# Performance work log

Measured on AMD Instinct MI355X. Metric: run time of the kernel, lower is better.

The kernel has to match this reference:

```python
import jax, jax.numpy as jnp
import numpy as np
from jax import lax

C = 256        # CONV_DIM / hidden size
VOC = 97       # VOC_SIZE + 1
T_DEC = 25     # NUM_CHARS
N = 512        # number of rois
H_IN, W_IN = 8, 32
GROUPS = 32    # GroupNorm groups (detectron2 'GN' default)


def setup_inputs() -> dict:
    key = jax.random.key(0)
    ks = jax.random.split(key, 16)
    nrm = lambda k, shp, s=0.05: jax.random.normal(k, shp, dtype=jnp.float32) * s
    inp = {}
    inp['rois'] = jax.random.normal(ks[0], (N, C, H_IN, W_IN), dtype=jnp.float32)
    inp['targets'] = jax.random.randint(ks[1], (N, T_DEC), 0, VOC)
    inp['conv1_w'] = nrm(ks[2], (C, C, 3, 3))
    inp['gn1_s'] = jnp.ones((C,), jnp.float32); inp['gn1_b'] = jnp.zeros((C,), jnp.float32)
    inp['conv2_w'] = nrm(ks[3], (C, C, 3, 3))
    inp['gn2_s'] = jnp.ones((C,), jnp.float32); inp['gn2_b'] = jnp.zeros((C,), jnp.float32)
    inp['lstm_wih_f'] = nrm(ks[4], (4 * C, C)); inp['lstm_whh_f'] = nrm(ks[5], (4 * C, C))
    inp['lstm_bih_f'] = jnp.zeros((4 * C,), jnp.float32); inp['lstm_bhh_f'] = jnp.zeros((4 * C,), jnp.float32)
    inp['lstm_wih_b'] = nrm(ks[6], (4 * C, C)); inp['lstm_whh_b'] = nrm(ks[7], (4 * C, C))
    inp['lstm_bih_b'] = jnp.zeros((4 * C,), jnp.float32); inp['lstm_bhh_b'] = jnp.zeros((4 * C,), jnp.float32)
    inp['emb_w'] = nrm(ks[8], (C, 2 * C)); inp['emb_b'] = jnp.zeros((C,), jnp.float32)
    inp['att_emb'] = nrm(ks[9], (VOC, C), 1.0)
    inp['comb_w'] = nrm(ks[10], (C, 2 * C)); inp['comb_b'] = jnp.zeros((C,), jnp.float32)
    inp['gru_wih'] = nrm(ks[11], (3 * C, C)); inp['gru_whh'] = nrm(ks[12], (3 * C, C))
    inp['gru_bih'] = jnp.zeros((3 * C,), jnp.float32); inp['gru_bhh'] = jnp.zeros((3 * C,), jnp.float32)
    inp['out_w'] = nrm(ks[13], (VOC, C)); inp['out_b'] = jnp.zeros((VOC,), jnp.float32)
    inp['vat_w'] = nrm(ks[14], (1, C)); inp['vat_b'] = jnp.zeros((1,), jnp.float32)
    return inp


def group_norm(x, scale, bias, groups=GROUPS, eps=1e-5):
    n, c, h, w = x.shape
    xg = x.reshape(n, groups, c // groups, h, w)
    mu = xg.mean(axis=(2, 3, 4), keepdims=True)
    var = xg.var(axis=(2, 3, 4), keepdims=True)
    xg = (xg - mu) * lax.rsqrt(var + eps)
    return xg.reshape(n, c, h, w) * scale[None, :, None, None] + bias[None, :, None, None]


def lstm_dir(xs, w_ih, w_hh, b_ih, b_hh, reverse):
    # xs: (T, N, C); PyTorch LSTM gate order i, f, g, o
    n = xs.shape[1]; hdim = w_hh.shape[1]
    def step(carry, x):
        h, c = carry
        g = x @ w_ih.T + b_ih + h @ w_hh.T + b_hh
        i, f, gg, o = jnp.split(g, 4, axis=-1)
        c = jax.nn.sigmoid(f) * c + jax.nn.sigmoid(i) * jnp.tanh(gg)
        h = jax.nn.sigmoid(o) * jnp.tanh(c)
        return (h, c), h
    z = jnp.zeros((n, hdim), xs.dtype)
    _, hs = lax.scan(step, (z, z), xs, reverse=reverse)
    return hs


def reference(rois, targets, conv1_w, gn1_s, gn1_b, conv2_w, gn2_s, gn2_b,
              lstm_wih_f, lstm_whh_f, lstm_bih_f, lstm_bhh_f,
              lstm_wih_b, lstm_whh_b, lstm_bih_b, lstm_bhh_b,
              emb_w, emb_b, att_emb, comb_w, comb_b,
              gru_wih, gru_whh, gru_bih, gru_bhh, out_w, out_b, vat_w, vat_b):
    # ---- CRNN encoder ----
    def conv_gn_relu(x, w, s, b):
        y = lax.conv_general_dilated(x, w, window_strides=(2, 1),
                                     padding=((1, 1), (1, 1)),
                                     dimension_numbers=('NCHW', 'OIHW', 'NCHW'))
        return jax.nn.relu(group_norm(y, s, b))
    x = conv_gn_relu(rois, conv1_w, gn1_s, gn1_b)
    x = conv_gn_relu(x, conv2_w, gn2_s, gn2_b)
    x = x.mean(axis=2).transpose(2, 0, 1)            # (T=W, N, C)
    hf = lstm_dir(x, lstm_wih_f, lstm_whh_f, lstm_bih_f, lstm_bhh_f, False)
    hb = lstm_dir(x, lstm_wih_b, lstm_whh_b, lstm_bih_b, lstm_bhh_b, True)
    enc = jnp.concatenate([hf, hb], axis=-1) @ emb_w.T + emb_b   # (T, N, C)

    # ---- attention GRU decoder (training path, deterministic teacher forcing) ----
    n = enc.shape[1]
    dec_in = jnp.concatenate([jnp.zeros((n, 1), targets.dtype), targets[:, :-1]], axis=1).T  # (T_DEC, N)
    dec_tgt = targets.T                                                                        # (T_DEC, N)

    def dec_step(h, inp):
        tok, tgt = inp                       # (N,), (N,)
        emb = att_emb[tok]                   # (N, C); dropout disabled
        alpha = jnp.tanh(h[None] + enc)      # (T, N, C)
        scores = jnp.einsum('tnc,c->tn', alpha, vat_w[0]) + vat_b[0]
        aw = jax.nn.softmax(scores, axis=0)  # softmax over encoder time
        ctx = jnp.einsum('tn,tnc->nc', aw, enc)
        xin = jax.nn.relu(jnp.concatenate([emb, ctx], axis=1) @ comb_w.T + comb_b)
        gi = xin @ gru_wih.T + gru_bih
        gh = h @ gru_whh.T + gru_bhh
        ir, iz, inn = jnp.split(gi, 3, axis=1)
        hr, hz, hn = jnp.split(gh, 3, axis=1)
        r = jax.nn.sigmoid(ir + hr)
        z = jax.nn.sigmoid(iz + hz)
        ng = jnp.tanh(inn + r * hn)
        h_new = (1.0 - z) * ng + z * h
        logp = jax.nn.log_softmax(h_new @ out_w.T + out_b, axis=1)
        step_loss = -jnp.mean(jnp.take_along_axis(logp, tgt[:, None], axis=1))
        return h_new, step_loss

    h0 = jnp.zeros((n, C), enc.dtype)
    _, losses = lax.scan(dec_step, h0, (dec_in, dec_tgt))
    return losses.sum()
```

## Files before the change

kernel.cpp:

```cpp
#include <hip/hip_runtime.h>
#include <math.h>

#define NROI 512
#define CDIM 256
#define TENC 32
#define TDEC 25
#define VOCC 97

typedef unsigned short ushort_t;
typedef unsigned char uchar_t;
typedef __attribute__((ext_vector_type(8))) short short8v;
typedef __attribute__((ext_vector_type(4))) float float4v;

__device__ __forceinline__ float sigmoidf_(float x){
    x = fminf(fmaxf(x, -30.f), 30.f);
    return __builtin_amdgcn_rcpf(1.f + __expf(-x));
}
__device__ __forceinline__ float tanhf_(float x){
    x = fminf(fmaxf(x, -15.f), 15.f);
    float e = __expf(2.f * x);
    return (e - 1.f) * __builtin_amdgcn_rcpf(e + 1.f);
}
__device__ __forceinline__ ushort_t f2b(float f){
    unsigned u = __float_as_uint(f);
    u = u + 0x7fffu + ((u >> 16) & 1u);
    return (ushort_t)(u >> 16);
}
__device__ __forceinline__ float b2f(ushort_t h){
    return __uint_as_float(((unsigned)h) << 16);
}
__device__ __forceinline__ uchar_t f2fp8(float x){
    x = fminf(fmaxf(x, -448.f), 448.f);
    int p = __builtin_amdgcn_cvt_pk_fp8_f32(x, x, 0, false);
    return (uchar_t)(p & 0xff);
}

__global__ void convert_all_k(
    const float* c1s, const float* c2s, const float* wf, const float* wb,
    const float* hf, const float* hb, const float* em, const float* cb,
    const float* gi, const float* gh, const float* ow, const float* ob,
    const float* bif, const float* bhf, const float* bib, const float* bhb,
    ushort_t* d_c1, ushort_t* d_c2, ushort_t* d_wf, ushort_t* d_wb,
    uchar_t* d_hf8, uchar_t* d_hb8, ushort_t* d_em,
    ushort_t* d_cwL, uchar_t* d_cwR8,
    uchar_t* d_gi8, uchar_t* d_gh8, ushort_t* d_ow, float* d_ob,
    float* d_b2f, float* d_b2b)
{
    int i = blockIdx.x * 256 + threadIdx.x;
    if (i < 589824) {
        int co = i / 2304, rem = i % 2304, tap = rem >> 8, ci = rem & 255;
        d_c1[i] = f2b(c1s[co * 2304 + ci * 9 + tap]); return;
    }
    i -= 589824;
    if (i < 589824) {
        int co = i / 2304, rem = i % 2304, tap = rem >> 8, ci = rem & 255;
        d_c2[i] = f2b(c2s[co * 2304 + ci * 9 + tap]); return;
    }
    i -= 589824;
    if (i < 262144) { d_wf[i] = f2b(wf[i]); return; }  i -= 262144;
    if (i < 262144) { d_wb[i] = f2b(wb[i]); return; }  i -= 262144;
    if (i < 262144) { d_hf8[i] = f2fp8(hf[i]); return; }  i -= 262144;
    if (i < 262144) { d_hb8[i] = f2fp8(hb[i]); return; }  i -= 262144;
    if (i < 131072) { d_em[i] = f2b(em[i]); return; }  i -= 131072;
    if (i < 131072) {
        int col = i >> 9, rest = i & 511;
        float v = cb[i];
        if (rest < 256) d_cwL[col * 256 + rest] = f2b(v);
        else            d_cwR8[col * 256 + (rest - 256)] = f2fp8(v);
        return;
    }
    i -= 131072;
    if (i < 196608) { d_gi8[i] = f2fp8(gi[i]); return; }  i -= 196608;
    if (i < 196608) { d_gh8[i] = f2fp8(gh[i]); return; }  i -= 196608;
    if (i < 32768) {
        int r = i >> 8;
        d_ow[i] = (r < VOCC) ? f2b(ow[i - (r << 8) + r * 256]) : 0; return;
    }
    i -= 32768;
    if (i < 128) { d_ob[i] = (i < VOCC) ? ob[i] : 0.f; return; }  i -= 128;
    if (i < 1024) { d_b2f[i] = bif[i] + bhf[i]; return; }  i -= 1024;
    if (i < 1024) { d_b2b[i] = bib[i] + bhb[i]; return; }
}

__global__ void nchw2nhwc_k(const float* __restrict__ in, ushort_t* __restrict__ out)
{
    __shared__ float t[64][33];
    int b = blockIdx.x;
    int cb = b & 3, h = (b >> 2) & 7, n = b >> 5;
    const float* src = in + (((size_t)n * 256 + cb * 64) * 8 + h) * 32;
    int w = threadIdx.x & 31, cr = threadIdx.x >> 5;
    #pragma unroll
    for (int p = 0; p < 8; p++) {
        int c = p * 8 + cr;
        t[c][w] = src[(size_t)c * 256 + w];
    }
    __syncthreads();
    int c2 = threadIdx.x & 63, wr2 = threadIdx.x >> 6;
    ushort_t* dst = out + ((size_t)n * 8 + h) * 32 * 256 + cb * 64;
    #pragma unroll
    for (int q = 0; q < 8; q++) {
        int ww = q * 4 + wr2;
        dst[(size_t)ww * 256 + c2] = f2b(t[c2][ww]);
    }
}

__global__ void emb_gather_k(const int* __restrict__ targets, const float* __restrict__ att_emb,
                             ushort_t* __restrict__ EMB)
{
    int idx = blockIdx.x * 256 + threadIdx.x;
    int c = idx & 255;
    int n = (idx >> 8) & 511;
    int t = idx >> 17;
    int tok = (t == 0) ? 0 : targets[n * TDEC + t - 1];
    EMB[idx] = f2b(att_emb[tok * 256 + c]);
}

template<int OUTBF, int ACT>
__global__ void __launch_bounds__(256, 2)
mgemm_k(const ushort_t* __restrict__ A, const ushort_t* __restrict__ B,
        const float* __restrict__ bias, void* __restrict__ Cout,
        int M, int N, int K)
{
    __shared__ ushort_t As[128 * 40];
    __shared__ ushort_t Bs[128 * 40];
    const int tid = threadIdx.x;
    const int lane = tid & 63, wid = tid >> 6;
    const int wr = wid >> 1, wc = wid & 1;
    const int bm = blockIdx.y * 128, bn = blockIdx.x * 128;

    const int r0 = tid >> 2, c0 = tid & 3;
    const int r1 = r0 + 64;
    const size_t Ar0 = (size_t)(bm + r0) * K, Ar1 = (size_t)(bm + r1) * K;
    const size_t Br0 = (size_t)(bn + r0) * K, Br1 = (size_t)(bn + r1) * K;

    float4v acc[4][4];
    #pragma unroll
    for (int m = 0; m < 4; m++)
        #pragma unroll
        for (int n = 0; n < 4; n++) { float4v z = {0.f,0.f,0.f,0.f}; acc[m][n] = z; }

    short8v ra[2][2], rb[2][2];
    auto LOAD = [&](int b, int k0) {
        ra[b][0] = *(const short8v*)&A[Ar0 + k0 + c0 * 8];
        ra[b][1] = *(const short8v*)&A[Ar1 + k0 + c0 * 8];
        rb[b][0] = *(const short8v*)&B[Br0 + k0 + c0 * 8];
        rb[b][1] = *(const short8v*)&B[Br1 + k0 + c0 * 8];
    };
    auto STORE = [&](int b) {
        *(short8v*)&As[r0 * 40 + c0 * 8] = ra[b][0];
        *(short8v*)&As[r1 * 40 + c0 * 8] = ra[b][1];
        *(short8v*)&Bs[r0 * 40 + c0 * 8] = rb[b][0];
        *(short8v*)&Bs[r1 * 40 + c0 * 8] = rb[b][1];
    };
    const int lr = lane & 15, lk = lane >> 4;
    auto COMPUTE = [&]() {
        short8v af[4], bf[4];
        #pragma unroll
        for (int m = 0; m < 4; m++)
            af[m] = *(const short8v*)&As[(wr * 64 + m * 16 + lr) * 40 + lk * 8];
        #pragma unroll
        for (int n = 0; n < 4; n++)
            bf[n] = *(const short8v*)&Bs[(wc * 64 + n * 16 + lr) * 40 + lk * 8];
        #pragma unroll
        for (int m = 0; m < 4; m++)
            #pragma unroll
            for (int n = 0; n < 4; n++)
                acc[m][n] = __builtin_amdgcn_mfma_f32_16x16x32_bf16(af[m], bf[n], acc[m][n], 0, 0, 0);
    };

    LOAD(0, 0);
    for (int k0 = 0; k0 < K; k0 += 64) {
        __syncthreads();
        STORE(0);
        __syncthreads();
        LOAD(1, k0 + 32);
        COMPUTE();
        __syncthreads();
        STORE(1);
        __syncthreads();
        if (k0 + 64 < K) LOAD(0, k0 + 64);
        COMPUTE();
    }

    #pragma unroll
    for (int m = 0; m < 4; m++)
        #pragma unroll
        for (int n = 0; n < 4; n++)
            #pragma unroll
            for (int r = 0; r < 4; r++) {
                int row = bm + wr * 64 + m * 16 + lk * 4 + r;
                int col = bn + wc * 64 + n * 16 + lr;
                float v = acc[m][n][r];
                if (bias) v += bias[col];
                if (ACT == 1) v = fmaxf(v, 0.f);
                if (OUTBF) ((ushort_t*)Cout)[(size_t)row * N + col] = f2b(v);
                else       ((float*)   Cout)[(size_t)row * N + col] = v;
            }
}

__global__ void __launch_bounds__(256, 2)
cgemm_k(const ushort_t* __restrict__ in, const ushort_t* __restrict__ wt,
        ushort_t* __restrict__ out, int Hin, int hmask, int nshift)
{
    const int K = 2304;
    __shared__ ushort_t As[128 * 40];
    __shared__ ushort_t Bs[256 * 40];
    const int tid = threadIdx.x;
    const int lane = tid & 63, wv = tid >> 6;
    const int byy = (blockIdx.y & 7) * (gridDim.y >> 3) + (blockIdx.y >> 3);
    const int bm = byy * 128;

    const int r0 = tid >> 2, c0 = tid & 3;
    const int r1 = r0 + 64;
    const int row0 = bm + r0, row1 = bm + r1;
    const int wo0 = row0 & 31, wo1 = row1 & 31;
    const int hh0 = ((row0 >> 5) & hmask) * 2 - 1, hh1 = ((row1 >> 5) & hmask) * 2 - 1;
    const size_t base0 = (size_t)(row0 >> nshift) * Hin * 32 * 256;
    const size_t base1 = (size_t)(row1 >> nshift) * Hin * 32 * 256;
    size_t Br[4];
    #pragma unroll
    for (int j = 0; j < 4; j++) Br[j] = (size_t)(r0 + j * 64) * K;

    float4v acc[8][4];
    #pragma unroll
    for (int m = 0; m < 8; m++)
        #pragma unroll
        for (int n = 0; n < 4; n++) { float4v z = {0.f,0.f,0.f,0.f}; acc[m][n] = z; }

    short8v ra[2][2], rb[2][4];
    const short8v zv = {0,0,0,0,0,0,0,0};
    auto LOAD = [&](int b, int k0) {
        int tap = k0 >> 8;
        int kh = tap / 3, kw = tap - kh * 3;
        int ci = (k0 & 255) + c0 * 8;
        int hi0 = hh0 + kh, wi0 = wo0 - 1 + kw;
        int hi1 = hh1 + kh, wi1 = wo1 - 1 + kw;
        ra[b][0] = ((unsigned)hi0 < (unsigned)Hin && (unsigned)wi0 < 32u)
                 ? *(const short8v*)&in[base0 + ((size_t)hi0 * 32 + wi0) * 256 + ci] : zv;
        ra[b][1] = ((unsigned)hi1 < (unsigned)Hin && (unsigned)wi1 < 32u)
                 ? *(const short8v*)&in[base1 + ((size_t)hi1 * 32 + wi1) * 256 + ci] : zv;
        #pragma unroll
        for (int j = 0; j < 4; j++)
            rb[b][j] = *(const short8v*)&wt[Br[j] + k0 + c0 * 8];
    };
    auto STORE = [&](int b) {
        *(short8v*)&As[r0 * 40 + c0 * 8] = ra[b][0];
        *(short8v*)&As[r1 * 40 + c0 * 8] = ra[b][1];
        #pragma unroll
        for (int j = 0; j < 4; j++)
            *(short8v*)&Bs[(r0 + j * 64) * 40 + c0 * 8] = rb[b][j];
    };
    const int lr = lane & 15, lk = lane >> 4;
    auto COMPUTE = [&]() {
        short8v af[8];
        #pragma unroll
        for (int m = 0; m < 8; m++)
            af[m] = *(const short8v*)&As[(m * 16 + lr) * 40 + lk * 8];
        #pragma unroll
        for (int n = 0; n < 4; n++) {
            short8v bf = *(const short8v*)&Bs[(wv * 64 + n * 16 + lr) * 40 + lk * 8];
            #pragma unroll
            for (int m = 0; m < 8; m++)
                acc[m][n] = __builtin_amdgcn_mfma_f32_16x16x32_bf16(af[m], bf, acc[m][n], 0, 0, 0);
        }
    };

    LOAD(0, 0);
    for (int k0 = 0; k0 < K; k0 += 64) {
        __syncthreads();
        STORE(0);
        __syncthreads();
        LOAD(1, k0 + 32);
        COMPUTE();
        __syncthreads();
        STORE(1);
        __syncthreads();
        if (k0 + 64 < K) LOAD(0, k0 + 64);
        COMPUTE();
    }

    #pragma unroll
    for (int m = 0; m < 8; m++)
        #pragma unroll
        for (int n = 0; n < 4; n++)
            #pragma unroll
            for (int r = 0; r < 4; r++) {
                int row = bm + m * 16 + lk * 4 + r;
                int col = wv * 64 + n * 16 + lr;
                out[(size_t)row * 256 + col] = f2b(acc[m][n][r]);
            }
}

__device__ __forceinline__ void gn_stats(float sum, float sq, int len,
                                         float* rs, float* rq, float& mu, float& rstd)
{
    for (int o = 32; o > 0; o >>= 1) { sum += __shfl_down(sum, o); sq += __shfl_down(sq, o); }
    int wid = threadIdx.x >> 6, lane = threadIdx.x & 63;
    if (lane == 0) { rs[wid] = sum; rq[wid] = sq; }
    __syncthreads();
    if (threadIdx.x == 0) {
        float S = rs[0] + rs[1] + rs[2] + rs[3];
        float Q = rq[0] + rq[1] + rq[2] + rq[3];
        float m = S / len;
        rs[4] = m; rq[4] = rsqrtf(Q / len - m * m + 1e-5f);
    }
    __syncthreads();
    mu = rs[4]; rstd = rq[4];
}

__global__ void gn_nhwc_k(const ushort_t* __restrict__ y, ushort_t* __restrict__ x,
                          const float* __restrict__ s, const float* __restrict__ b, int HW)
{
    __shared__ float rs[8], rq[8];
    int blk = blockIdx.x; int g = blk & 31; int n = blk >> 5;
    const ushort_t* p = y + (size_t)n * HW * 256 + g * 8;
    ushort_t* q = x + (size_t)n * HW * 256 + g * 8;
    int len = HW * 8;
    float sum = 0.f, sq = 0.f;
    for (int e = threadIdx.x; e < len; e += 256) {
        int hw = e >> 3, c = e & 7;
        float v = b2f(p[hw * 256 + c]);
        sum += v; sq += v * v;
    }
    float mu, rstd;
    gn_stats(sum, sq, len, rs, rq, mu, rstd);
    for (int e = threadIdx.x; e < len; e += 256) {
        int hw = e >> 3, c = e & 7;
        float v = (b2f(p[hw * 256 + c]) - mu) * rstd * s[g * 8 + c] + b[g * 8 + c];
        q[hw * 256 + c] = f2b(fmaxf(v, 0.f));
    }
}

__global__ void gn_pool_k(const ushort_t* __restrict__ y, ushort_t* __restrict__ xT,
                          const float* __restrict__ s, const float* __restrict__ b)
{
    __shared__ float rs[8], rq[8];
    int blk = blockIdx.x; int g = blk & 31; int n = blk >> 5;
    const ushort_t* p = y + (size_t)n * 64 * 256 + g * 8;
    float sum = 0.f, sq = 0.f;
    for (int e = threadIdx.x; e < 512; e += 256) {
        int hw = e >> 3, c = e & 7;
        float v = b2f(p[hw * 256 + c]);
        sum += v; sq += v * v;
    }
    float mu, rstd;
    gn_stats(sum, sq, 512, rs, rq, mu, rstd);
    int w = threadIdx.x >> 3, c = threadIdx.x & 7;
    float sc = s[g * 8 + c], bb = b[g * 8 + c];
    float v0 = (b2f(p[(size_t)w * 256 + c]) - mu) * rstd * sc + bb;
    float v1 = (b2f(p[(size_t)(32 + w) * 256 + c]) - mu) * rstd * sc + bb;
    float pooled = 0.5f * (fmaxf(v0, 0.f) + fmaxf(v1, 0.f));
    xT[((size_t)w * 512 + n) * 256 + g * 8 + c] = f2b(pooled);
}

__global__ void __launch_bounds__(512, 1)
lstm_persist_k(const ushort_t* __restrict__ XG,
               const uchar_t* __restrict__ whF8, const uchar_t* __restrict__ whB8,
               ushort_t* __restrict__ hcat)
{
    __shared__ __align__(16) uchar_t hf8[16][264];
    __shared__ float gL[16][1028];
    const int blk = blockIdx.x;
    const int dir = blk >> 5;
    const int r0  = (blk & 31) * 16;
    const uchar_t* W = dir ? whB8 : whF8;
    const int tid = threadIdx.x, lane = tid & 63, wv = tid >> 6;
    const int lr = lane & 15, lk = lane >> 4;
    const float4v z4 = {0.f, 0.f, 0.f, 0.f};

    long pw[8][8];
    #pragma unroll
    for (int j = 0; j < 8; j++) {
        int col0 = (j * 8 + wv) * 16;
        #pragma unroll
        for (int kf = 0; kf < 8; kf++)
            pw[j][kf] = *(const long*)&W[(size_t)(col0 + lr) * 256 + kf * 32 + lk * 8];
    }

    for (int i = tid; i < 16 * 264; i += 512) ((uchar_t*)hf8)[i] = 0;
    float creg[8];
    #pragma unroll
    for (int r = 0; r < 8; r++) creg[r] = 0.f;
    const int ccol = tid & 255;
    const int rbase = (tid >> 8) * 8;
    __syncthreads();

    for (int s = 0; s < TENC; s++) {
        int t = dir ? (31 - s) : s;
        float xga[8][4];
        #pragma unroll
        for (int j = 0; j < 8; j++) {
            int col = (j * 8 + wv) * 16 + lr;
            #pragma unroll
            for (int r = 0; r < 4; r++)
                xga[j][r] = b2f(XG[(size_t)t * 1048576 +
                                   (size_t)(r0 + lk * 4 + r) * 2048 + dir * 1024 + col]);
        }
        long aH[8];
        #pragma unroll
        for (int kf = 0; kf < 8; kf++)
            aH[kf] = *(const long*)&hf8[lr][kf * 32 + lk * 8];
        #pragma unroll
        for (int j = 0; j < 8; j++) {
            int col = (j * 8 + wv) * 16 + lr;
            float4v acc = z4;
            #pragma unroll
            for (int kf = 0; kf < 8; kf++)
                acc = __builtin_amdgcn_mfma_f32_16x16x32_fp8_fp8(aH[kf], pw[j][kf], acc, 0, 0, 0);
            #pragma unroll
            for (int r = 0; r < 4; r++)
                gL[lk * 4 + r][col] = acc[r] + xga[j][r];
        }
        __syncthreads();
        #pragma unroll
        for (int rr = 0; rr < 8; rr++) {
            int row = rbase + rr;
            float i_ = sigmoidf_(gL[row][ccol]);
            float f_ = sigmoidf_(gL[row][256 + ccol]);
            float g_ = tanhf_(gL[row][512 + ccol]);
            float o_ = sigmoidf_(gL[row][768 + ccol]);
            float cn = f_ * creg[rr] + i_ * g_;
            creg[rr] = cn;
            float hn = o_ * tanhf_(cn);
            hf8[row][ccol] = f2fp8(hn);
            hcat[((size_t)t * 512 + (r0 + row)) * 512 + dir * 256 + ccol] = f2b(hn);
        }
        __syncthreads();
    }
}

__global__ void __launch_bounds__(512, 1)
dec_local_k(const ushort_t* __restrict__ enc, const ushort_t* __restrict__ xinpre,
            const uchar_t* __restrict__ cwR8, const uchar_t* __restrict__ gwih8,
            const uchar_t* __restrict__ gwhh8, const float* __restrict__ gbih,
            const float* __restrict__ gbhh, const float* __restrict__ vw,
            const float* __restrict__ vb, ushort_t* __restrict__ hist)
{
    __shared__ ushort_t encL[2][32][264];
    __shared__ __align__(16) uchar_t cwL8[16 * 8 * 64 * 8];
    __shared__ float    hL[2][256];
    __shared__ __align__(16) uchar_t hf8[2][264];
    __shared__ __align__(16) uchar_t xf8[2][264];
    __shared__ __align__(16) uchar_t ctx8[2][264];
    __shared__ float    giL[2][776];
    __shared__ float    ghL[2][776];
    __shared__ float    scl[2][32];

    const int tid = threadIdx.x, lane = tid & 63, wv = tid >> 6;
    const int nbase = blockIdx.x * 2;
    const int lr = lane & 15, lk = lane >> 4;
    const float4v z4 = {0.f,0.f,0.f,0.f};

    for (int i = tid; i < 2 * 256; i += 512) hL[i >> 8][i & 255] = 0.f;
    for (int i = tid; i < 2 * 264; i += 512) hf8[i / 264][i % 264] = 0;
    for (int v = tid; v < 2048; v += 512) {
        int r = v >> 10;
        int rem = v & 1023;
        int t2 = rem >> 5;
        int c8 = (rem & 31) * 8;
        *(short8v*)&encL[r][t2][c8] =
            *(const short8v*)&enc[((size_t)t2 * 512 + nbase + r) * 256 + c8];
    }
    #pragma unroll
    for (int q = 0; q < 2; q++) {
        int tile = wv * 2 + q;
        int col0 = tile * 16;
        #pragma unroll
        for (int kf = 0; kf < 8; kf++) {
            long v = *(const long*)&cwR8[(size_t)(col0 + lr) * 256 + kf * 32 + lk * 8];
            *(long*)&cwL8[((tile * 8 + kf) * 64 + lane) * 8] = v;
        }
    }
    long pgh[6][8], pgi[6][8];
    #pragma unroll
    for (int j = 0; j < 6; j++) {
        int col0 = (j * 8 + wv) * 16;
        #pragma unroll
        for (int kf = 0; kf < 8; kf++) {
            pgh[j][kf] = *(const long*)&gwhh8[(size_t)(col0 + lr) * 256 + kf * 32 + lk * 8];
            pgi[j][kf] = *(const long*)&gwih8[(size_t)(col0 + lr) * 256 + kf * 32 + lk * 8];
        }
    }
    __syncthreads();

    float vwreg[4];
    #pragma unroll
    for (int j = 0; j < 4; j++) vwreg[j] = vw[lane + 64 * j];
    const float vbias = vb[0];
    float gbh_r[6], gbi_r[6];
    #pragma unroll
    for (int j = 0; j < 6; j++) {
        int col0 = (j * 8 + wv) * 16;
        gbh_r[j] = gbhh[col0 + lr];
        gbi_r[j] = gbih[col0 + lr];
    }

    for (int t = 0; t < TDEC; t++) {
        float xp[2][2];
        #pragma unroll
        for (int q = 0; q < 2; q++) {
            int col0 = (wv * 2 + q) * 16;
            xp[q][0] = b2f(xinpre[(size_t)t * 131072 + (size_t)(nbase + 0) * 256 + col0 + lr]);
            xp[q][1] = b2f(xinpre[(size_t)t * 131072 + (size_t)(nbase + 1) * 256 + col0 + lr]);
        }
        float4v ghacc[6];
        {
            long aH[8];
            #pragma unroll
            for (int kf = 0; kf < 8; kf++)
                aH[kf] = (lr < 2) ? *(const long*)&hf8[lr][kf * 32 + lk * 8] : 0L;
            #pragma unroll
            for (int j = 0; j < 6; j++) {
                float4v acc = z4;
                #pragma unroll
                for (int kf = 0; kf < 8; kf++)
                    acc = __builtin_amdgcn_mfma_f32_16x16x32_fp8_fp8(aH[kf], pgh[j][kf], acc, 0, 0, 0);
                ghacc[j] = acc;
            }
        }
        {
            int r = wv >> 2;
            int t2b = (wv & 3) * 8;
            float hreg[4];
            #pragma unroll
            for (int j = 0; j < 4; j++) hreg[j] = hL[r][lane + 64 * j];
            #pragma unroll
            for (int q = 0; q < 8; q++) {
                int t2 = t2b + q;
                float s = 0.f;
                #pragma unroll
                for (int j = 0; j < 4; j++)
                    s += tanhf_(hreg[j] + b2f(encL[r][t2][lane + 64 * j])) * vwreg[j];
                for (int o = 32; o > 0; o >>= 1) s += __shfl_down(s, o);
                if (lane == 0) scl[r][t2] = s + vbias;
            }
        }
        if (lk == 0) {
            #pragma unroll
            for (int j = 0; j < 6; j++) {
                int col0 = (j * 8 + wv) * 16;
                ghL[0][col0 + lr] = ghacc[j][0] + gbh_r[j];
                ghL[1][col0 + lr] = ghacc[j][1] + gbh_r[j];
            }
        }
        __syncthreads();
        {
            int r = tid >> 8, c = tid & 255;
            float m = -1e30f;
            #pragma unroll
            for (int t2 = 0; t2 < 32; t2++) m = fmaxf(m, scl[r][t2]);
            float ssum = 0.f, acc = 0.f;
            #pragma unroll 8
            for (int t2 = 0; t2 < 32; t2++) {
                float e = __expf(scl[r][t2] - m);
                ssum += e;
                acc += e * b2f(encL[r][t2][c]);
            }
            ctx8[r][c] = f2fp8(acc * __builtin_amdgcn_rcpf(ssum));
        }
        __syncthreads();
        {
            long aC[8];
            #pragma unroll
            for (int kf = 0; kf < 8; kf++)
                aC[kf] = (lr < 2) ? *(const long*)&ctx8[lr][kf * 32 + lk * 8] : 0L;
            #pragma unroll
            for (int q = 0; q < 2; q++) {
                int tile = wv * 2 + q;
                int col0 = tile * 16;
                float4v acc = z4;
                #pragma unroll
                for (int kf = 0; kf < 8; kf++) {
                    long b = *(const long*)&cwL8[((tile * 8 + kf) * 64 + lane) * 8];
                    acc = __builtin_amdgcn_mfma_f32_16x16x32_fp8_fp8(aC[kf], b, acc, 0, 0, 0);
                }
                if (lk == 0) {
                    xf8[0][col0 + lr] = f2fp8(fmaxf(acc[0] + xp[q][0], 0.f));
                    xf8[1][col0 + lr] = f2fp8(fmaxf(acc[1] + xp[q][1], 0.f));
                }
            }
        }
        __syncthreads();
        {
            long aX[8];
            #pragma unroll
            for (int kf = 0; kf < 8; kf++)
                aX[kf] = (lr < 2) ? *(const long*)&xf8[lr][kf * 32 + lk * 8] : 0L;
            #pragma unroll
            for (int j = 0; j < 6; j++) {
                int col0 = (j * 8 + wv) * 16;
                float4v acc = z4;
                #pragma unroll
                for (int kf = 0; kf < 8; kf++)
                    acc = __builtin_amdgcn_mfma_f32_16x16x32_fp8_fp8(aX[kf], pgi[j][kf], acc, 0, 0, 0);
                if (lk == 0) {
                    giL[0][col0 + lr] = acc[0] + gbi_r[j];
                    giL[1][col0 + lr] = acc[1] + gbi_r[j];
                }
            }
        }
        __syncthreads();
        {
            int r = tid >> 8, c = tid & 255;
            float rg = sigmoidf_(giL[r][c] + ghL[r][c]);
            float zg = sigmoidf_(giL[r][256 + c] + ghL[r][256 + c]);
            float ng = tanhf_(giL[r][512 + c] + rg * ghL[r][512 + c]);
            float hv = (1.f - zg) * ng + zg * hL[r][c];
            hL[r][c] = hv;
            hf8[r][c] = f2fp8(hv);
            __builtin_nontemporal_store(f2b(hv), &hist[((size_t)t * 512 + nbase + r) * 256 + c]);
        }
        __syncthreads();
    }
}

__global__ void loss_batch_k(const float* __restrict__ logits, const int* __restrict__ targets,
                             float* __restrict__ part)
{
    __shared__ float red[256];
    int t = blockIdx.x;
    float acc = 0.f;
    for (int rr = threadIdx.x; rr < 512; rr += 256) {
        const float* row = logits + ((size_t)t * 512 + rr) * 128;
        float m = -1e30f;
        for (int j = 0; j < VOCC; j++) m = fmaxf(m, row[j]);
        float s2 = 0.f;
        for (int j = 0; j < VOCC; j++) s2 += __expf(row[j] - m);
        int tg = targets[rr * TDEC + t];
        acc += m + __logf(s2) - row[tg];
    }
    red[threadIdx.x] = acc;
    __syncthreads();
    for (int o = 128; o > 0; o >>= 1) {
        if (threadIdx.x < o) red[threadIdx.x] += red[threadIdx.x + o];
        __syncthreads();
    }
    if (threadIdx.x == 0) part[t] = red[0] / 512.f;
}

__global__ void loss_final_k(const float* __restrict__ part, float* __restrict__ out)
{
    if (threadIdx.x == 0) {
        float s = 0.f;
        for (int t = 0; t < TDEC; t++) s += part[t];
        out[0] = s;
    }
}

extern "C" void kernel_launch(void* const* d_in, const int* in_sizes, int n_in,
                              void* d_out, int out_size, void* d_ws, size_t ws_size,
                              hipStream_t stream)
{
    const float* rois     = (const float*)d_in[0];
    const int*   targets  = (const int*)  d_in[1];
    const float* conv1_w  = (const float*)d_in[2];
    const float* gn1_s    = (const float*)d_in[3];
    const float* gn1_b    = (const float*)d_in[4];
    const float* conv2_w  = (const float*)d_in[5];
    const float* gn2_s    = (const float*)d_in[6];
    const float* gn2_b    = (const float*)d_in[7];
    const float* wih_f    = (const float*)d_in[8];
    const float* whh_f    = (const float*)d_in[9];
    const float* bih_f    = (const float*)d_in[10];
    const float* bhh_f    = (const float*)d_in[11];
    const float* wih_b    = (const float*)d_in[12];
    const float* whh_b    = (const float*)d_in[13];
    const float* bih_b    = (const float*)d_in[14];
    const float* bhh_b    = (const float*)d_in[15];
    const float* emb_w    = (const float*)d_in[16];
    const float* emb_b    = (const float*)d_in[17];
    const float* att_emb  = (const float*)d_in[18];
    const float* comb_w   = (const float*)d_in[19];
    const float* comb_b   = (const float*)d_in[20];
    const float* gru_wih  = (const float*)d_in[21];
    const float* gru_whh  = (const float*)d_in[22];
    const float* gru_bih  = (const float*)d_in[23];
    const float* gru_bhh  = (const float*)d_in[24];
    const float* out_w    = (const float*)d_in[25];
    const float* out_b    = (const float*)d_in[26];
    const float* vat_w    = (const float*)d_in[27];
    const float* vat_b    = (const float*)d_in[28];

    float* ws = (float*)d_ws;
    const size_t REG1 = 0;
    const size_t REG2 = 16777216;
    const size_t REG3 = 25165824;
    const size_t WREG = 33554432;

    ushort_t* R      = (ushort_t*)(ws + REG1);
    ushort_t* xg     = (ushort_t*)(ws + REG1);
    ushort_t* EMB    = (ushort_t*)(ws + REG1);
    ushort_t* xinpre = (ushort_t*)(ws + REG1 + 1638400);

    ushort_t* Y1b    = (ushort_t*)(ws + REG2);
    ushort_t* Y2b    = (ushort_t*)(ws + REG2);
    ushort_t* xT     = (ushort_t*)(ws + REG2 + 4194304);
    ushort_t* hcat   = (ushort_t*)(ws + REG2);
    ushort_t* X1b    = (ushort_t*)(ws + REG3);
    ushort_t* enc    = (ushort_t*)(ws + REG3);
    ushort_t* hist   = (ushort_t*)(ws + REG3 + 2097152);
    float*    logitsA= ws + REG3 + 3735552;
    float*    lpart  = ws + REG3 + 5373952;

    ushort_t* c1w    = (ushort_t*)(ws + WREG);
    ushort_t* c2w    = (ushort_t*)(ws + WREG + 294912);
    ushort_t* wihf   = (ushort_t*)(ws + WREG + 589824);
    uchar_t*  whhf8  = (uchar_t*) (ws + WREG + 851968);
    uchar_t*  whhb8  = (uchar_t*) (ws + WREG + 917504);
    ushort_t* embw   = (ushort_t*)(ws + WREG + 1114112);
    ushort_t* cwL    = (ushort_t*)(ws + WREG + 1179648);
    uchar_t*  cwR8   = (uchar_t*) (ws + WREG + 1212416);
    uchar_t*  gwih8  = (uchar_t*) (ws + WREG + 1245184);
    uchar_t*  gwhh8  = (uchar_t*) (ws + WREG + 1294336);
    ushort_t* outw   = (ushort_t*)(ws + WREG + 1343488);
    float*    outb   = ws + WREG + 1359872;
    float*    bias2f = ws + WREG + 1360000;
    float*    bias2b = ws + WREG + 1361024;

    dim3 blk(256);

    convert_all_k<<<11402, blk, 0, stream>>>(
        conv1_w, conv2_w, wih_f, wih_b, whh_f, whh_b, emb_w, comb_w,
        gru_wih, gru_whh, out_w, out_b, bih_f, bhh_f, bih_b, bhh_b,
        c1w, c2w, wihf, (ushort_t*)(ws + WREG + 720896), whhf8, whhb8, embw,
        cwL, cwR8, gwih8, gwhh8, outw, outb, bias2f, bias2b);

    nchw2nhwc_k<<<16384, blk, 0, stream>>>(rois, R);
    cgemm_k<<<dim3(1, 512), blk, 0, stream>>>(R, c1w, Y1b, 8, 3, 7);
    gn_nhwc_k<<<16384, blk, 0, stream>>>(Y1b, X1b, gn1_s, gn1_b, 128);
    cgemm_k<<<dim3(1, 256), blk, 0, stream>>>(X1b, c2w, Y2b, 4, 1, 6);
    gn_pool_k<<<16384, blk, 0, stream>>>(Y2b, xT, gn2_s, gn2_b);

    mgemm_k<1,0><<<dim3(16, 128), blk, 0, stream>>>(xT, wihf, bias2f, xg, 16384, 2048, 256);

    lstm_persist_k<<<64, dim3(512), 0, stream>>>(xg, whhf8, whhb8, hcat);

    mgemm_k<1,0><<<dim3(2, 128), blk, 0, stream>>>(hcat, embw, emb_b, enc, 16384, 256, 512);

    emb_gather_k<<<12800, blk, 0, stream>>>(targets, att_emb, EMB);
    mgemm_k<1,0><<<dim3(2, 100), blk, 0, stream>>>(EMB, cwL, comb_b, xinpre, 12800, 256, 256);

    dec_local_k<<<256, dim3(512), 0, stream>>>(enc, xinpre, cwR8, gwih8, gwhh8,
        gru_bih, gru_bhh, vat_w, vat_b, hist);

    mgemm_k<0,0><<<dim3(1, 100), blk, 0, stream>>>(hist, outw, outb, logitsA, 12800, 128, 256);
    loss_batch_k<<<TDEC, blk, 0, stream>>>(logitsA, targets, lpart);
    loss_final_k<<<1, dim3(64), 0, stream>>>(lpart, (float*)d_out);
}
```

Measured before the change: 826.1 us.

## Fuse GroupNorm, ReLU and pooling into conv GEMM epilogues

Moves the GroupNorm statistics, normalization, ReLU and, for the second conv, the height pooling and transpose into the conv GEMM epilogue, computing group stats with wave shuffles over the accumulator tile. This removes two standalone GN kernels and their round-trips of the conv outputs through global memory. It depends on each 128-row block holding whole images and each group's 8 channels sitting in one wave's lanes, and it adds register pressure to the epilogue.

Result: faster. 719.3 us (-12.9%).

```diff
diff --git a/kernel.cpp b/kernel.cpp
--- a/kernel.cpp
+++ b/kernel.cpp
@@ -198,8 +198,10 @@
             }
 }
 
+template<int CONV2>
 __global__ void __launch_bounds__(256, 2)
-cgemm_k(const ushort_t* __restrict__ in, const ushort_t* __restrict__ wt,
+convf_k(const ushort_t* __restrict__ in, const ushort_t* __restrict__ wt,
+        const float* __restrict__ gns, const float* __restrict__ gnb,
         ushort_t* __restrict__ out, int Hin, int hmask, int nshift)
 {
     const int K = 2304;
@@ -279,78 +281,84 @@
         COMPUTE();
     }
 
-    #pragma unroll
-    for (int m = 0; m < 8; m++)
-        #pragma unroll
-        for (int n = 0; n < 4; n++)
-            #pragma unroll
-            for (int r = 0; r < 4; r++) {
-                int row = bm + m * 16 + lk * 4 + r;
-                int col = wv * 64 + n * 16 + lr;
-                out[(size_t)row * 256 + col] = f2b(acc[m][n][r]);
+    float sc_[4], bb_[4];
+    #pragma unroll
+    for (int nn = 0; nn < 4; nn++) {
+        int col = wv * 64 + nn * 16 + lr;
+        sc_[nn] = gns[col];
+        bb_[nn] = gnb[col];
+    }
+
+    if (CONV2 == 0) {
+        float mu_[4], rs_[4];
+        #pragma unroll
+        for (int nn = 0; nn < 4; nn++) {
+            float s = 0.f, q = 0.f;
+            #pragma unroll
+            for (int m = 0; m < 8; m++)
+                #pragma unroll
+                for (int r = 0; r < 4; r++) { float v = acc[m][nn][r]; s += v; q += v * v; }
+            s += __shfl_xor(s, 16); q += __shfl_xor(q, 16);
+            s += __shfl_xor(s, 32); q += __shfl_xor(q, 32);
+            s += __shfl_xor(s, 1);  q += __shfl_xor(q, 1);
+            s += __shfl_xor(s, 2);  q += __shfl_xor(q, 2);
+            s += __shfl_xor(s, 4);  q += __shfl_xor(q, 4);
+            float mu = s * (1.f / 1024.f);
+            mu_[nn] = mu;
+            rs_[nn] = rsqrtf(q * (1.f / 1024.f) - mu * mu + 1e-5f);
+        }
+        #pragma unroll
+        for (int m = 0; m < 8; m++)
+            #pragma unroll
+            for (int nn = 0; nn < 4; nn++)
+                #pragma unroll
+                for (int r = 0; r < 4; r++) {
+                    int row = bm + m * 16 + lk * 4 + r;
+                    int col = wv * 64 + nn * 16 + lr;
+                    float v = (acc[m][nn][r] - mu_[nn]) * rs_[nn] * sc_[nn] + bb_[nn];
+                    out[(size_t)row * 256 + col] = f2b(fmaxf(v, 0.f));
+                }
+    } else {
+        float mu_[2][4], rs_[2][4];
+        #pragma unroll
+        for (int img = 0; img < 2; img++)
+            #pragma unroll
+            for (int nn = 0; nn < 4; nn++) {
+                float s = 0.f, q = 0.f;
+                #pragma unroll
+                for (int m2 = 0; m2 < 4; m2++)
+                    #pragma unroll
+                    for (int r = 0; r < 4; r++) {
+                        float v = acc[img * 4 + m2][nn][r]; s += v; q += v * v;
+                    }
+                s += __shfl_xor(s, 16); q += __shfl_xor(q, 16);
+                s += __shfl_xor(s, 32); q += __shfl_xor(q, 32);
+                s += __shfl_xor(s, 1);  q += __shfl_xor(q, 1);
+                s += __shfl_xor(s, 2);  q += __shfl_xor(q, 2);
+                s += __shfl_xor(s, 4);  q += __shfl_xor(q, 4);
+                float mu = s * (1.f / 512.f);
+                mu_[img][nn] = mu;
+                rs_[img][nn] = rsqrtf(q * (1.f / 512.f) - mu * mu + 1e-5f);
             }
-}
-
-__device__ __forceinline__ void gn_stats(float sum, float sq, int len,
-                                         float* rs, float* rq, float& mu, float& rstd)
-{
-    for (int o = 32; o > 0; o >>= 1) { sum += __shfl_down(sum, o); sq += __shfl_down(sq, o); }
-    int wid = threadIdx.x >> 6, lane = threadIdx.x & 63;
-    if (lane == 0) { rs[wid] = sum; rq[wid] = sq; }
-    __syncthreads();
-    if (threadIdx.x == 0) {
-        float S = rs[0] + rs[1] + rs[2] + rs[3];
-        float Q = rq[0] + rq[1] + rq[2] + rq[3];
-        float m = S / len;
-        rs[4] = m; rq[4] = rsqrtf(Q / len - m * m + 1e-5f);
-    }
-    __syncthreads();
-    mu = rs[4]; rstd = rq[4];
-}
-
-__global__ void gn_nhwc_k(const ushort_t* __restrict__ y, ushort_t* __restrict__ x,
-                          const float* __restrict__ s, const float* __restrict__ b, int HW)
-{
-    __shared__ float rs[8], rq[8];
-    int blk = blockIdx.x; int g = blk & 31; int n = blk >> 5;
-    const ushort_t* p = y + (size_t)n * HW * 256 + g * 8;
-    ushort_t* q = x + (size_t)n * HW * 256 + g * 8;
-    int len = HW * 8;
-    float sum = 0.f, sq = 0.f;
-    for (int e = threadIdx.x; e < len; e += 256) {
-        int hw = e >> 3, c = e & 7;
-        float v = b2f(p[hw * 256 + c]);
-        sum += v; sq += v * v;
-    }
-    float mu, rstd;
-    gn_stats(sum, sq, len, rs, rq, mu, rstd);
-    for (int e = threadIdx.x; e < len; e += 256) {
-        int hw = e >> 3, c = e & 7;
-        float v = (b2f(p[hw * 256 + c]) - mu) * rstd * s[g * 8 + c] + b[g * 8 + c];
-        q[hw * 256 + c] = f2b(fmaxf(v, 0.f));
-    }
-}
-
-__global__ void gn_pool_k(const ushort_t* __restrict__ y, ushort_t* __restrict__ xT,
-                          const float* __restrict__ s, const float* __restrict__ b)
-{
-    __shared__ float rs[8], rq[8];
-    int blk = blockIdx.x; int g = blk & 31; int n = blk >> 5;
-    const ushort_t* p = y + (size_t)n * 64 * 256 + g * 8;
-    float sum = 0.f, sq = 0.f;
-    for (int e = threadIdx.x; e < 512; e += 256) {
-        int hw = e >> 3, c = e & 7;
-        float v = b2f(p[hw * 256 + c]);
-        sum += v; sq += v * v;
-    }
-    float mu, rstd;
-    gn_stats(sum, sq, 512, rs, rq, mu, rstd);
-    int w = threadIdx.x >> 3, c = threadIdx.x & 7;
-    float sc = s[g * 8 + c], bb = b[g * 8 + c];
-    float v0 = (b2f(p[(size_t)w * 256 + c]) - mu) * rstd * sc + bb;
-    float v1 = (b2f(p[(size_t)(32 + w) * 256 + c]) - mu) * rstd * sc + bb;
-    float pooled = 0.5f * (fmaxf(v0, 0.f) + fmaxf(v1, 0.f));
-    xT[((size_t)w * 512 + n) * 256 + g * 8 + c] = f2b(pooled);
+        const int nimg0 = bm >> 6;
+        #pragma unroll
+        for (int img = 0; img < 2; img++)
+            #pragma unroll
+            for (int m2 = 0; m2 < 2; m2++)
+                #pragma unroll
+                for (int nn = 0; nn < 4; nn++)
+                    #pragma unroll
+                    for (int r = 0; r < 4; r++) {
+                        int m = img * 4 + m2;
+                        float v0 = (acc[m][nn][r]     - mu_[img][nn]) * rs_[img][nn] * sc_[nn] + bb_[nn];
+                        float v1 = (acc[m + 2][nn][r] - mu_[img][nn]) * rs_[img][nn] * sc_[nn] + bb_[nn];
+                        float pooled = 0.5f * (fmaxf(v0, 0.f) + fmaxf(v1, 0.f));
+                        int wo = m2 * 16 + lk * 4 + r;
+                        int nimg = nimg0 + img;
+                        int col = wv * 64 + nn * 16 + lr;
+                        out[((size_t)wo * 512 + nimg) * 256 + col] = f2b(pooled);
+                    }
+    }
 }
 
 __global__ void __launch_bounds__(512, 1)
@@ -692,8 +700,6 @@
     ushort_t* EMB    = (ushort_t*)(ws + REG1);
     ushort_t* xinpre = (ushort_t*)(ws + REG1 + 1638400);
 
-    ushort_t* Y1b    = (ushort_t*)(ws + REG2);
-    ushort_t* Y2b    = (ushort_t*)(ws + REG2);
     ushort_t* xT     = (ushort_t*)(ws + REG2 + 4194304);
     ushort_t* hcat   = (ushort_t*)(ws + REG2);
     ushort_t* X1b    = (ushort_t*)(ws + REG3);
@@ -726,10 +732,8 @@
         cwL, cwR8, gwih8, gwhh8, outw, outb, bias2f, bias2b);
 
     nchw2nhwc_k<<<16384, blk, 0, stream>>>(rois, R);
-    cgemm_k<<<dim3(1, 512), blk, 0, stream>>>(R, c1w, Y1b, 8, 3, 7);
-    gn_nhwc_k<<<16384, blk, 0, stream>>>(Y1b, X1b, gn1_s, gn1_b, 128);
-    cgemm_k<<<dim3(1, 256), blk, 0, stream>>>(X1b, c2w, Y2b, 4, 1, 6);
-    gn_pool_k<<<16384, blk, 0, stream>>>(Y2b, xT, gn2_s, gn2_b);
+    convf_k<0><<<dim3(1, 512), blk, 0, stream>>>(R, c1w, gn1_s, gn1_b, X1b, 8, 3, 7);
+    convf_k<1><<<dim3(1, 256), blk, 0, stream>>>(X1b, c2w, gn2_s, gn2_b, xT, 4, 1, 6);
 
     mgemm_k<1,0><<<dim3(16, 128), blk, 0, stream>>>(xT, wihf, bias2f, xg, 16384, 2048, 256);
 
```
